# Kernel optimization log

Measured on AMD Instinct MI355X. Metric: run time of the kernel, lower is better.

## Reference

```python
import jax, jax.numpy as jnp
import numpy as np

B, E, C = 256, 512, 256          # batch, entity_size, entity_embedding_size
AR, H256, H32 = 1024, 256, 32
NUM_ACTIONS, MAX_UNIT_TYPE = 564, 256
MAX_SELECTED = 64
TEMPERATURE = 1.0                # is_sl_training=True -> temperature forced to 1.0


def setup_inputs() -> dict:
    key = jax.random.key(0)
    ks = jax.random.split(key, 20)
    s = 0.02
    inp = {
        "autoregressive_embedding": jax.random.normal(ks[0], (B, AR), jnp.float32),
        "action_type": jax.random.randint(ks[1], (B, 1), 0, NUM_ACTIONS, jnp.int64),
        "entity_embeddings": jax.random.normal(ks[2], (B, E, C), jnp.float32),
        # func_embed Dense(max_unit_type -> 256)
        "Wf": jax.random.normal(ks[3], (MAX_UNIT_TYPE, H256)) * s,
        "bf": jnp.zeros((H256,)),
        # conv_1 Conv1D(kernel_size=1): C -> 32
        "Wk": jax.random.normal(ks[4], (C, H32)) * s,
        "bk": jnp.zeros((H32,)),
        # fc_1 Dense(AR -> 256)
        "W1": jax.random.normal(ks[5], (AR, H256)) * s,
        "b1": jnp.zeros((H256,)),
        # fc_2 Dense(256 -> 32)
        "W2": jax.random.normal(ks[6], (H256, H32)) * s,
        "b2": jnp.zeros((H32,)),
        # small_lstm: input 32 -> hidden 32, keras gate order (i, f, g, o)
        "Wx": jax.random.normal(ks[7], (H32, 4 * H32)) * s,
        "Wh": jax.random.normal(ks[8], (H32, 4 * H32)) * s,
        "bl": jnp.zeros((4 * H32,)),
        # project Dense(32 -> AR)
        "Wp": jax.random.normal(ks[9], (H32, AR)) * s,
        "bp": jnp.zeros((AR,)),
        # stand-ins for utils.action_can_apply_to_entity_types_mask / action_involve_selecting_units_mask
        "unit_mask_table": (jax.random.uniform(ks[10], (NUM_ACTIONS, MAX_UNIT_TYPE)) < 0.5).astype(jnp.float32),
        "select_table": (jax.random.uniform(ks[11], (NUM_ACTIONS,)) < 0.5).astype(jnp.float32),
    }
    return inp


def _lstm_step(x, h, c, Wx, Wh, bl):
    z = x @ Wx + h @ Wh + bl                       # [B, 4H]
    i, f, g, o = jnp.split(z, 4, axis=-1)
    i, f, o = jax.nn.sigmoid(i), jax.nn.sigmoid(f), jax.nn.sigmoid(o)
    c = f * c + i * jnp.tanh(g)
    h = o * jnp.tanh(c)
    return h, c


def reference(autoregressive_embedding, action_type, entity_embeddings,
              Wf, bf, Wk, bk, W1, b1, W2, b2, Wx, Wh, bl, Wp, bp,
              unit_mask_table, select_table):
    a = action_type[:, 0]                                          # [B]
    unit_types_one_hot = unit_mask_table[a]                        # [B, max_unit_type]
    the_func_embed = jax.nn.relu(unit_types_one_hot @ Wf + bf)     # [B, 256]
    key_proj = jnp.einsum('bec,ch->beh', entity_embeddings, Wk) + bk  # [B, E, 32]

    sample_key = jax.random.key(42)
    h0 = jnp.zeros((B, H32), entity_embeddings.dtype)
    c0 = jnp.zeros((B, H32), entity_embeddings.dtype)
    mask0 = jnp.ones((B, E), entity_embeddings.dtype)

    def body(carry, _):
        ar, mask, h, c, rng = carry
        x = ar @ W1 + b1                                           # fc_1
        z2 = jax.nn.relu(the_func_embed + x) @ W2 + b2             # fc_2, [B, 32]
        h, c = _lstm_step(z2, h, c, Wx, Wh, bl)                    # single LSTM step
        query = h                                                  # [B, 32]
        y = jnp.einsum('beh,bh->be', key_proj, query)              # attention scores
        y2 = y * jax.lax.stop_gradient(mask)
        entity_logits = y2 / TEMPERATURE                           # [B, E]
        entity_probs = jax.nn.softmax(entity_logits, axis=-1)
        rng, sub = jax.random.split(rng)
        # tf.random.categorical treats its input as logits -> Gumbel-argmax over entity_probs
        gumbel = -jnp.log(-jnp.log(jax.random.uniform(sub, (B, E), minval=1e-20, maxval=1.0)))
        entity_id = jnp.argmax(entity_probs + gumbel, axis=-1)     # [B]
        mask = mask.at[jnp.arange(B), entity_id].set(0.0)
        one_hot = jax.nn.one_hot(entity_id, E, dtype=key_proj.dtype)
        out = jnp.einsum('be,beh->bh', one_hot, key_proj)          # [B, 32]
        out = out - jnp.mean(one_hot, axis=-1, keepdims=True)
        ar = ar + (out @ Wp + bp)
        return (ar, mask, h, c, rng), (entity_logits, entity_id)

    (ar, _, _, _, _), (logits_seq, units_seq) = jax.lax.scan(
        body, (autoregressive_embedding, mask0, h0, c0, sample_key), None, length=MAX_SELECTED)

    units_logits = jnp.transpose(logits_seq, (1, 0, 2))            # [B, S, E]
    units = jnp.transpose(units_seq, (1, 0))[:, :, None]           # [B, S, 1]

    select = select_table[a][:, None]                              # [B, 1]
    units_logits = units_logits * select[:, :, None]
    units = units * select[:, :, None].astype(units.dtype)
    ar = ar * select
    return units_logits, units, ar
```

## Files before the change

### kernel.cpp

```cpp
#include <hip/hip_runtime.h>


#define JAX_PARTITIONABLE 1

typedef unsigned int u32;
typedef _Float16 half2v __attribute__((ext_vector_type(2)));

#define NB 256
#define NE 512
#define NT 64

#define OFF_UNITS 8388608
#define OFF_AR    8404992

#define WS_WQ   0
#define WS_CV   8192
#define WS_XF0  8448
#define WS_WK2  73984
#define WS_GU   78080

#define BARL() asm volatile("s_waitcnt lgkmcnt(0)\n\ts_barrier" ::: "memory")

struct U2 { u32 a, b; };

__host__ __device__ constexpr u32 rotl32(u32 x, int r) {
  return (x << r) | (x >> (32 - r));
}

__host__ __device__ constexpr U2 tf2x32(u32 k0, u32 k1, u32 x0, u32 x1) {
  u32 ks2 = k0 ^ k1 ^ 0x1BD11BDAu;
  x0 += k0; x1 += k1;
  x0 += x1; x1 = rotl32(x1, 13); x1 ^= x0;
  x0 += x1; x1 = rotl32(x1, 15); x1 ^= x0;
  x0 += x1; x1 = rotl32(x1, 26); x1 ^= x0;
  x0 += x1; x1 = rotl32(x1, 6);  x1 ^= x0;
  x0 += k1; x1 += ks2 + 1u;
  x0 += x1; x1 = rotl32(x1, 17); x1 ^= x0;
  x0 += x1; x1 = rotl32(x1, 29); x1 ^= x0;
  x0 += x1; x1 = rotl32(x1, 16); x1 ^= x0;
  x0 += x1; x1 = rotl32(x1, 24); x1 ^= x0;
  x0 += ks2; x1 += k0 + 2u;
  x0 += x1; x1 = rotl32(x1, 13); x1 ^= x0;
  x0 += x1; x1 = rotl32(x1, 15); x1 ^= x0;
  x0 += x1; x1 = rotl32(x1, 26); x1 ^= x0;
  x0 += x1; x1 = rotl32(x1, 6);  x1 ^= x0;
  x0 += k0; x1 += k1 + 3u;
  x0 += x1; x1 = rotl32(x1, 17); x1 ^= x0;
  x0 += x1; x1 = rotl32(x1, 29); x1 ^= x0;
  x0 += x1; x1 = rotl32(x1, 16); x1 ^= x0;
  x0 += x1; x1 = rotl32(x1, 24); x1 ^= x0;
  x0 += k1; x1 += ks2 + 4u;
  x0 += x1; x1 = rotl32(x1, 13); x1 ^= x0;
  x0 += x1; x1 = rotl32(x1, 15); x1 ^= x0;
  x0 += x1; x1 = rotl32(x1, 26); x1 ^= x0;
  x0 += x1; x1 = rotl32(x1, 6);  x1 ^= x0;
  x0 += ks2; x1 += k0 + 5u;
  return U2{x0, x1};
}

struct KeyTab { u32 s0[NT]; u32 s1[NT]; };

__host__ __device__ constexpr KeyTab make_tab() {
  KeyTab t{};
  u32 k0 = 0u, k1 = 42u;
  for (int i = 0; i < NT; ++i) {
#if JAX_PARTITIONABLE
    U2 nk = tf2x32(k0, k1, 0u, 0u);
    U2 sb = tf2x32(k0, k1, 0u, 1u);
#else
    U2 r02 = tf2x32(k0, k1, 0u, 2u);
    U2 r13 = tf2x32(k0, k1, 1u, 3u);
    U2 nk{r02.a, r13.a};
    U2 sb{r02.b, r13.b};
#endif
    t.s0[i] = sb.a; t.s1[i] = sb.b;
    k0 = nk.a; k1 = nk.b;
  }
  return t;
}

__constant__ KeyTab SUBTAB = make_tab();

__device__ __forceinline__ float gumbel_draw(u32 k0, u32 k1, u32 jf) {
#if JAX_PARTITIONABLE
  U2 v = tf2x32(k0, k1, 0u, jf);
  u32 bits = v.a ^ v.b;
#else
  u32 bits;
  if (jf < 65536u) { U2 v = tf2x32(k0, k1, jf, jf + 65536u); bits = v.a; }
  else             { U2 v = tf2x32(k0, k1, jf - 65536u, jf); bits = v.b; }
#endif
  float f = __uint_as_float((bits >> 9) | 0x3f800000u) - 1.0f;
  float u = f + 1e-20f;
  u = fmaxf(u, 1e-20f);
  return -__logf(-__logf(u));
}

__device__ __forceinline__ float fdot2f(half2v a, half2v b, float c) {
#if __has_builtin(__builtin_amdgcn_fdot2)
  return __builtin_amdgcn_fdot2(a, b, c, false);
#else
  return c + (float)a.x * (float)b.x + (float)a.y * (float)b.y;
#endif
}


__device__ __forceinline__ void amax_comb(float& v, int& i, float vo, int io) {
  if (vo > v || (vo == v && io < i)) { v = vo; i = io; }
}

__device__ __forceinline__ void amax_sh(float& v, int& i, int m) {
  float vo = __shfl_xor(v, m);
  int io = __shfl_xor(i, m);
  amax_comb(v, i, vo, io);
}

#if __has_builtin(__builtin_amdgcn_mov_dpp)
#define HAVE_DPP 1
template <int CTRL>
__device__ __forceinline__ void amax_dpp(float& v, int& i) {
  float vo = __int_as_float(
      __builtin_amdgcn_mov_dpp(__float_as_int(v), CTRL, 0xF, 0xF, true));
  int io = __builtin_amdgcn_mov_dpp(i, CTRL, 0xF, 0xF, true);
  amax_comb(v, i, vo, io);
}
#endif

__device__ __forceinline__ void wave_amax(float& v, int& i) {
#ifdef HAVE_DPP
  amax_dpp<0xB1>(v, i);
  amax_dpp<0x4E>(v, i);
  amax_dpp<0x124>(v, i);
  amax_dpp<0x128>(v, i);
  amax_sh(v, i, 16);
  amax_sh(v, i, 32);
#else
  #pragma unroll
  for (int s = 1; s < 64; s <<= 1) amax_sh(v, i, s);
#endif
}

__global__ __launch_bounds__(512) void suh_gum(
    const int* __restrict__ act, const float* __restrict__ selt,
    float* __restrict__ gws)
{
  const u32 blk = blockIdx.x;
  const int b = (int)(blk >> 6), step = (int)(blk & 63u);
  if (selt[act[b]] == 0.0f) return;
  const int e = threadIdx.x;
  gws[((size_t)blk << 9) | (u32)e] =
      gumbel_draw(SUBTAB.s0[step], SUBTAB.s1[step], (u32)(b * 512 + e));
}

__global__ __launch_bounds__(512) void suh_prep(
    const float* __restrict__ ar0, const int* __restrict__ act,
    const float* __restrict__ Wf, const float* __restrict__ bfv,
    const float* __restrict__ W1, const float* __restrict__ b1,
    const float* __restrict__ Wp, const float* __restrict__ bp,
    const float* __restrict__ Wk, const float* __restrict__ umt,
    float* __restrict__ ws)
{
  __shared__ float lvec[1024];
  __shared__ float red2[512];
  __shared__ float feL[256];
  __shared__ float lum[256];
  const int t = threadIdx.x;
  const int bid = blockIdx.x;

  if (bid >= 289) {
    half2v* wkp = (half2v*)(ws + WS_WK2);
    #pragma unroll
    for (int i = 0; i < 8; ++i) {
      const int p = t * 8 + i;
      const int c2 = p >> 5, h = p & 31;
      half2v v = { (_Float16)Wk[c2 * 64 + h], (_Float16)Wk[c2 * 64 + 32 + h] };
      wkp[p] = v;
    }
    return;
  }

  const int o = t & 255, hf = t >> 8;
  const float* src;
  if (bid < NB) src = ar0 + bid * 1024;
  else if (bid < NB + 32) src = Wp + (bid - NB) * 1024;
  else src = bp;

  for (int i = t; i < 1024; i += 512) lvec[i] = src[i];
  if (bid < NB && t < 256) lum[t] = umt[act[bid] * 256 + t];
  __syncthreads();

  float p = 0.0f;
  const int kb = hf * 512;
  #pragma unroll 16
  for (int k = 0; k < 512; ++k) p = fmaf(lvec[kb + k], W1[(kb + k) * 256 + o], p);
  red2[hf * 256 + o] = p;
  if (bid < NB && hf == 1) {
    float fe = bfv[o];
    #pragma unroll 8
    for (int k = 0; k < 256; ++k) fe = fmaf(lum[k], Wf[k * 256 + o], fe);
    feL[o] = fmaxf(fe, 0.0f);
  }
  __syncthreads();

  if (t < 256) {
    const float s = red2[t] + red2[256 + t];
    if (bid < NB)            ws[WS_XF0 + bid * 256 + t] = s + b1[t] + feL[t];
    else if (bid < NB + 32)  ws[WS_WQ + (bid - NB) * 256 + t] = s;
    else                     ws[WS_CV + t] = s;
  }
}

__global__ __launch_bounds__(512, 1) void suh_main(
    const float* __restrict__ ar0, const int* __restrict__ act,
    const float* __restrict__ emb, const float* __restrict__ bk,
    const float* __restrict__ W2, const float* __restrict__ b2,
    const float* __restrict__ Wx, const float* __restrict__ Wh,
    const float* __restrict__ bl, const float* __restrict__ Wp,
    const float* __restrict__ bp, const float* __restrict__ selt,
    const float* __restrict__ ws, const float* __restrict__ gws,
    const int use_pre, float* __restrict__ outp)
{
  const int b = blockIdx.x;
  const int t = threadIdx.x;
  const float sel = selt[act[b]];
  float* outL = outp;
  float* outU = outp + OFF_UNITS;
  float* outA = outp + OFF_AR;

  if (sel == 0.0f) {
    float4 z4 = {0.0f, 0.0f, 0.0f, 0.0f};
    float4* pl = (float4*)(outL + (size_t)b * 32768);
    for (int i = t; i < 8192; i += 512) pl[i] = z4;
    if (t < 16) ((float4*)(outU + b * 64))[t] = z4;
    if (t < 256) ((float4*)(outA + b * 1024))[t] = z4;
    return;
  }

  __shared__ half2v kpT[16][NE];
  __shared__ float wq[32][256];
  __shared__ float xf[256];
  __shared__ float red[512];
  __shared__ float cvs[256];
  __shared__ float sacc[32];
  __shared__ half2v h2b[16];
  __shared__ float wsum[8];
  __shared__ float wargv[8];
  __shared__ int   wargi[8];

  const int hh = t & 31, kc = t >> 5;
  float w2r[16];
  #pragma unroll
  for (int i = 0; i < 16; ++i) w2r[i] = W2[(kc * 16 + i) * 32 + hh];

  float blv0 = 0.0f, blv1 = 0.0f, b2v = 0.0f;
  float hv = 0.0f, cv = 0.0f;
  if (t < 64) { blv0 = bl[t]; blv1 = bl[64 + t]; b2v = b2[t & 31]; }

  half2v w0r[32], w1r[32];
  if (t < 64) {
    #pragma unroll
    for (int r = 0; r < 32; ++r) {
      w0r[r] = half2v{ (_Float16)Wx[r * 128 + t],      (_Float16)Wh[r * 128 + t] };
      w1r[r] = half2v{ (_Float16)Wx[r * 128 + 64 + t], (_Float16)Wh[r * 128 + 64 + t] };
    }
  }

  {
    const float4* s4 = (const float4*)(ws + WS_WQ);
    float4* d4 = (float4*)&wq[0][0];
    for (int i = t; i < 2048; i += 512) d4[i] = s4[i];
  }
  if (t < 256) { xf[t] = ws[WS_XF0 + b * 256 + t]; cvs[t] = ws[WS_CV + t]; }
  if (t < 32) sacc[t] = 0.0f;
  float mymask = 1.0f;

  half2v kpr[16];
  {
    float acc[32];
    #pragma unroll
    for (int h = 0; h < 32; ++h) acc[h] = bk[h];
    const float4* erow = (const float4*)(emb + (size_t)b * (NE * 256) + (size_t)t * 256);
    const half2v* wkg = (const half2v*)(ws + WS_WK2);
    for (int c4 = 0; c4 < 64; ++c4) {
      float4 ev = erow[c4];
      half2v e01 = { (_Float16)ev.x, (_Float16)ev.y };
      half2v e23 = { (_Float16)ev.z, (_Float16)ev.w };
      const half2v* w0 = wkg + (2 * c4) * 32;
      const half2v* w1 = w0 + 32;
      #pragma unroll
      for (int h = 0; h < 32; ++h) {
        acc[h] = fdot2f(e01, w0[h], acc[h]);
        acc[h] = fdot2f(e23, w1[h], acc[h]);
      }
    }
    #pragma unroll
    for (int j = 0; j < 16; ++j) {
      half2v v = { (_Float16)acc[2 * j], (_Float16)acc[2 * j + 1] };
      kpr[j] = v;
      kpT[j][t] = v;
    }
  }
  __syncthreads();

  const size_t gbase = (size_t)b * 64 * 512 + t;

  for (int step = 0; step < NT; ++step) {
    float gum;
    if (use_pre) gum = gws[gbase + (size_t)step * 512];
    else gum = gumbel_draw(SUBTAB.s0[step], SUBTAB.s1[step], (u32)(b * 512 + t));

    {
      float pa = 0.0f;
      const float* xk = &xf[kc * 16];
      #pragma unroll
      for (int i = 0; i < 16; ++i) pa = fmaf(fmaxf(xk[i], 0.0f), w2r[i], pa);
      red[kc * 32 + hh] = pa;
    }
    BARL();

    if (t < 64) {
      const int h = t & 31, half = t >> 5;
      float z = 0.0f;
      #pragma unroll
      for (int i = 0; i < 8; ++i) z += red[(half * 8 + i) * 32 + h];
      z += __shfl_xor(z, 32);
      const float z2v = z + b2v;

      float g0 = blv0, g1 = blv1;
      #pragma unroll
      for (int r = 0; r < 32; ++r) {
        const float zr = __shfl(z2v, r);
        const float hr = __shfl(hv, r);
        half2v p0 = w0r[r];
        half2v p1 = w1r[r];
        g0 = fmaf(zr, (float)p0.x, g0); g0 = fmaf(hr, (float)p0.y, g0);
        g1 = fmaf(zr, (float)p1.x, g1); g1 = fmaf(hr, (float)p1.y, g1);
      }
      const float zf = __shfl_xor(g0, 32);
      const float zo = __shfl_xor(g1, 32);
      if (t < 32) {
        const float si = 1.0f / (1.0f + __expf(-g0));
        const float sf = 1.0f / (1.0f + __expf(-zf));
        const float so = 1.0f / (1.0f + __expf(-zo));
        cv = sf * cv + si * tanhf(g1);
        hv = so * tanhf(cv);
      }
      const float ha = __shfl(hv, 2 * (t & 31));
      const float hb = __shfl(hv, 2 * (t & 31) + 1);
      if (t < 16) { half2v v = { (_Float16)ha, (_Float16)hb }; h2b[t] = v; }
    }
    BARL();

    float a0 = 0.0f, a1 = 0.0f, a2 = 0.0f, a3 = 0.0f;
    #pragma unroll
    for (int j = 0; j < 16; j += 4) {
      a0 = fdot2f(kpr[j],     h2b[j],     a0);
      a1 = fdot2f(kpr[j + 1], h2b[j + 1], a1);
      a2 = fdot2f(kpr[j + 2], h2b[j + 2], a2);
      a3 = fdot2f(kpr[j + 3], h2b[j + 3], a3);
    }
    const float y2 = ((a0 + a1) + (a2 + a3)) * mymask;
    outL[(size_t)b * 32768 + step * 512 + t] = y2;
    const float ev = __expf(y2);
    float sv = ev;
    #pragma unroll
    for (int s = 1; s < 64; s <<= 1) sv += __shfl_xor(sv, s);
    if ((t & 63) == 0) wsum[t >> 6] = sv;
    BARL();

    float Z = wsum[0];
    #pragma unroll
    for (int i = 1; i < 8; ++i) Z += wsum[i];
    float val = ev / Z + gum;
    int idx = t;
    wave_amax(val, idx);
    if ((t & 63) == 0) { wargv[t >> 6] = val; wargi[t >> 6] = idx; }
    BARL();

    float bvv = wargv[0]; int id = wargi[0];
    #pragma unroll
    for (int i = 1; i < 8; ++i) {
      if (wargv[i] > bvv || (wargv[i] == bvv && wargi[i] < id)) { bvv = wargv[i]; id = wargi[i]; }
    }

    if (t == id) mymask = 0.0f;
    if (t == 0) outU[b * 64 + step] = (float)id;
    if (t < 32) {
      half2v kj = kpT[t >> 1][id];
      const float kv = (t & 1) ? (float)kj.y : (float)kj.x;
      sacc[t] += kv - 0.001953125f;
    }
    if (t < 256) {
      float dx = cvs[t];
      #pragma unroll
      for (int j = 0; j < 16; ++j) {
        half2v kj = kpT[j][id];
        dx = fmaf((float)kj.x - 0.001953125f, wq[2 * j][t], dx);
        dx = fmaf((float)kj.y - 0.001953125f, wq[2 * j + 1][t], dx);
      }
      xf[t] += dx;
    }
    BARL();
  }

  for (int j = t; j < 1024; j += 512) {
    float acc2 = ar0[b * 1024 + j] + 64.0f * bp[j];
    #pragma unroll 8
    for (int r = 0; r < 32; ++r) acc2 = fmaf(sacc[r], Wp[r * 1024 + j], acc2);
    outA[b * 1024 + j] = acc2;
  }
}

extern "C" void kernel_launch(void* const* d_in, const int* in_sizes, int n_in,
                              void* d_out, int out_size, void* d_ws, size_t ws_size,
                              hipStream_t stream)
{
  (void)in_sizes; (void)n_in; (void)out_size;
  const float* ar0 = (const float*)d_in[0];
  const int*   act = (const int*)d_in[1];
  const float* emb = (const float*)d_in[2];
  const float* Wf  = (const float*)d_in[3];
  const float* bfv = (const float*)d_in[4];
  const float* Wk  = (const float*)d_in[5];
  const float* bk  = (const float*)d_in[6];
  const float* W1  = (const float*)d_in[7];
  const float* b1  = (const float*)d_in[8];
  const float* W2  = (const float*)d_in[9];
  const float* b2  = (const float*)d_in[10];
  const float* Wx  = (const float*)d_in[11];
  const float* Wh  = (const float*)d_in[12];
  const float* bl  = (const float*)d_in[13];
  const float* Wp  = (const float*)d_in[14];
  const float* bp  = (const float*)d_in[15];
  const float* umt = (const float*)d_in[16];
  const float* selt = (const float*)d_in[17];
  float* ws = (float*)d_ws;
  float* outp = (float*)d_out;

  const size_t need = (size_t)(WS_GU + 8388608) * sizeof(float);
  const int use_pre = (ws_size >= need) ? 1 : 0;

  suh_prep<<<dim3(290), dim3(512), 0, stream>>>(ar0, act, Wf, bfv, W1, b1, Wp, bp, Wk, umt, ws);
  if (use_pre)
    suh_gum<<<dim3(16384), dim3(512), 0, stream>>>(act, selt, ws + WS_GU);
  suh_main<<<dim3(256), dim3(512), 0, stream>>>(ar0, act, emb, bk, W2, b2, Wx, Wh,
                                                bl, Wp, bp, selt, ws, ws + WS_GU,
                                                use_pre, outp);
}
```

Before: 531.8 us.

## Generate Gumbel noise in main loop during LSTM phase instead of precomputing

Drops the separate Gumbel precompute kernel and its 32 MB workspace round trip. Threads 64..511, which sit idle while the first wave runs the LSTM step, now draw the Gumbel noise inside the main loop, and a few of them also draw the first wave's values into shared memory. The change also swaps the LSTM broadcast shuffles for readlane and uses a DPP-based wave sum for the softmax denominator. The cost is extra Threefry and log work per step inside the serial loop, which only pays off if it hides under the LSTM critical path.

```diff
diff --git a/kernel.cpp b/kernel.cpp
--- a/kernel.cpp
+++ b/kernel.cpp
@@ -17,7 +17,6 @@
 #define WS_CV   8192
 #define WS_XF0  8448
 #define WS_WK2  73984
-#define WS_GU   78080
 
 #define BARL() asm volatile("s_waitcnt lgkmcnt(0)\n\ts_barrier" ::: "memory")
 
@@ -104,6 +103,14 @@
 #endif
 }
 
+__device__ __forceinline__ float rlf(float x, int l) {
+#if __has_builtin(__builtin_amdgcn_readlane)
+  return __int_as_float(__builtin_amdgcn_readlane(__float_as_int(x), l));
+#else
+  return __shfl(x, l);
+#endif
+}
+
 
 __device__ __forceinline__ void amax_comb(float& v, int& i, float vo, int io) {
   if (vo > v || (vo == v && io < i)) { v = vo; i = io; }
@@ -124,6 +131,11 @@
   int io = __builtin_amdgcn_mov_dpp(i, CTRL, 0xF, 0xF, true);
   amax_comb(v, i, vo, io);
 }
+template <int CTRL>
+__device__ __forceinline__ float dpp_addf(float x) {
+  return x + __int_as_float(
+      __builtin_amdgcn_mov_dpp(__float_as_int(x), CTRL, 0xF, 0xF, true));
+}
 #endif
 
 __device__ __forceinline__ void wave_amax(float& v, int& i) {
@@ -140,16 +152,19 @@
 #endif
 }
 
-__global__ __launch_bounds__(512) void suh_gum(
-    const int* __restrict__ act, const float* __restrict__ selt,
-    float* __restrict__ gws)
-{
-  const u32 blk = blockIdx.x;
-  const int b = (int)(blk >> 6), step = (int)(blk & 63u);
-  if (selt[act[b]] == 0.0f) return;
-  const int e = threadIdx.x;
-  gws[((size_t)blk << 9) | (u32)e] =
-      gumbel_draw(SUBTAB.s0[step], SUBTAB.s1[step], (u32)(b * 512 + e));
+__device__ __forceinline__ float wave_sum(float x) {
+#ifdef HAVE_DPP
+  x = dpp_addf<0xB1>(x);
+  x = dpp_addf<0x4E>(x);
+  x = dpp_addf<0x124>(x);
+  x = dpp_addf<0x128>(x);
+  x += __shfl_xor(x, 16);
+  x += __shfl_xor(x, 32);
+#else
+  #pragma unroll
+  for (int s = 1; s < 64; s <<= 1) x += __shfl_xor(x, s);
+#endif
+  return x;
 }
 
 __global__ __launch_bounds__(512) void suh_prep(
@@ -217,8 +232,7 @@
     const float* __restrict__ Wx, const float* __restrict__ Wh,
     const float* __restrict__ bl, const float* __restrict__ Wp,
     const float* __restrict__ bp, const float* __restrict__ selt,
-    const float* __restrict__ ws, const float* __restrict__ gws,
-    const int use_pre, float* __restrict__ outp)
+    const float* __restrict__ ws, float* __restrict__ outp)
 {
   const int b = blockIdx.x;
   const int t = threadIdx.x;
@@ -243,6 +257,7 @@
   __shared__ float cvs[256];
   __shared__ float sacc[32];
   __shared__ half2v h2b[16];
+  __shared__ float gumL[64];
   __shared__ float wsum[8];
   __shared__ float wargv[8];
   __shared__ int   wargi[8];
@@ -302,13 +317,7 @@
   }
   __syncthreads();
 
-  const size_t gbase = (size_t)b * 64 * 512 + t;
-
   for (int step = 0; step < NT; ++step) {
-    float gum;
-    if (use_pre) gum = gws[gbase + (size_t)step * 512];
-    else gum = gumbel_draw(SUBTAB.s0[step], SUBTAB.s1[step], (u32)(b * 512 + t));
-
     {
       float pa = 0.0f;
       const float* xk = &xf[kc * 16];
@@ -329,8 +338,8 @@
       float g0 = blv0, g1 = blv1;
       #pragma unroll
       for (int r = 0; r < 32; ++r) {
-        const float zr = __shfl(z2v, r);
-        const float hr = __shfl(hv, r);
+        const float zr = rlf(z2v, r);
+        const float hr = rlf(hv, r);
         half2v p0 = w0r[r];
         half2v p1 = w1r[r];
         g0 = fmaf(zr, (float)p0.x, g0); g0 = fmaf(hr, (float)p0.y, g0);
@@ -349,6 +358,14 @@
       const float hb = __shfl(hv, 2 * (t & 31) + 1);
       if (t < 16) { half2v v = { (_Float16)ha, (_Float16)hb }; h2b[t] = v; }
     }
+
+    float gum = 0.0f;
+    if (t >= 64) {
+      gum = gumbel_draw(SUBTAB.s0[step], SUBTAB.s1[step], (u32)(b * 512 + t));
+      if (t < 128)
+        gumL[t - 64] = gumbel_draw(SUBTAB.s0[step], SUBTAB.s1[step],
+                                   (u32)(b * 512 + (t - 64)));
+    }
     BARL();
 
     float a0 = 0.0f, a1 = 0.0f, a2 = 0.0f, a3 = 0.0f;
@@ -362,12 +379,11 @@
     const float y2 = ((a0 + a1) + (a2 + a3)) * mymask;
     outL[(size_t)b * 32768 + step * 512 + t] = y2;
     const float ev = __expf(y2);
-    float sv = ev;
-    #pragma unroll
-    for (int s = 1; s < 64; s <<= 1) sv += __shfl_xor(sv, s);
+    float sv = wave_sum(ev);
     if ((t & 63) == 0) wsum[t >> 6] = sv;
     BARL();
 
+    if (t < 64) gum = gumL[t];
     float Z = wsum[0];
     #pragma unroll
     for (int i = 1; i < 8; ++i) Z += wsum[i];
@@ -415,7 +431,7 @@
                               void* d_out, int out_size, void* d_ws, size_t ws_size,
                               hipStream_t stream)
 {
-  (void)in_sizes; (void)n_in; (void)out_size;
+  (void)in_sizes; (void)n_in; (void)out_size; (void)ws_size;
   const float* ar0 = (const float*)d_in[0];
   const int*   act = (const int*)d_in[1];
   const float* emb = (const float*)d_in[2];
@@ -437,13 +453,7 @@
   float* ws = (float*)d_ws;
   float* outp = (float*)d_out;
 
-  const size_t need = (size_t)(WS_GU + 8388608) * sizeof(float);
-  const int use_pre = (ws_size >= need) ? 1 : 0;
-
   suh_prep<<<dim3(290), dim3(512), 0, stream>>>(ar0, act, Wf, bfv, W1, b1, Wp, bp, Wk, umt, ws);
-  if (use_pre)
-    suh_gum<<<dim3(16384), dim3(512), 0, stream>>>(act, selt, ws + WS_GU);
   suh_main<<<dim3(256), dim3(512), 0, stream>>>(ar0, act, emb, bk, W2, b2, Wx, Wh,
-                                                bl, Wp, bp, selt, ws, ws + WS_GU,
-                                                use_pre, outp);
-}
+                                                bl, Wp, bp, selt, ws, outp);
+}
```

After: 484.5 us. 8.9% less time.
